# Kernel tuning notes

Hardware: AMD Instinct MI355X
Metric: run time of the kernel (lower is better)

## Reference

```python
import jax, jax.numpy as jnp
from jax import lax
import numpy as np

B, H, W = 128, 64, 64
L_I, L_H, L_Q, K = 3, 150, 16, 30
DN = ('NCHW', 'OIHW', 'NCHW')


def conv(x, w):
    return lax.conv_general_dilated(x, w, (1, 1), 'SAME', dimension_numbers=DN)


def setup_inputs() -> dict:
    key = jax.random.key(0)
    ks = jax.random.split(key, 10)
    return {
        'layout': jax.random.normal(ks[0], (B, 2, H, W), jnp.float32),
        'heatmap': jax.random.uniform(ks[1], (B, 1, H, W), jnp.float32),
        'h_w': jax.random.normal(ks[2], (L_H, L_I, 3, 3), jnp.float32) * 0.1,
        'h_b': jax.random.normal(ks[3], (L_H,), jnp.float32) * 0.1,
        'r_w': jax.random.normal(ks[4], (1, L_H, 1, 1), jnp.float32) * 0.1,
        'q_w': jax.random.normal(ks[5], (L_Q, 1, 3, 3), jnp.float32) * 0.1,
        'w': jax.random.normal(ks[6], (L_Q, 1, 3, 3), jnp.float32) * 0.1,
        'fc_w': jax.random.normal(ks[7], (4, L_Q), jnp.float32) * 0.1,
        'S1': jax.random.randint(ks[8], (B,), 0, H, jnp.int64),
        'S2': jax.random.randint(ks[9], (B,), 0, W, jnp.int64),
    }


def reference(layout, heatmap, h_w, h_b, r_w, q_w, w, fc_w, S1, S2):
    # X: [B, l_i, H, W]
    X = jnp.concatenate([layout, heatmap], axis=1)
    h = conv(X, h_w) + h_b[None, :, None, None]      # [B, l_h, H, W]
    r = conv(h, r_w)                                  # [B, 1, H, W]
    q = conv(r, q_w)                                  # [B, l_q, H, W]
    v = jnp.max(q, axis=1, keepdims=True)             # [B, 1, H, W]
    wq = jnp.concatenate([q_w, w], axis=1)            # [l_q, 2, 3, 3]

    def step(v, _):
        q = conv(jnp.concatenate([r, v], axis=1), wq)
        return jnp.max(q, axis=1, keepdims=True), None

    v, _ = lax.scan(step, v, None, length=K - 1)
    q = conv(jnp.concatenate([r, v], axis=1), wq)     # [B, l_q, H, W]

    b = jnp.arange(q.shape[0])
    q_out = q[b, :, S1, S2]                           # [B, l_q]
    logits = q_out @ fc_w.T                           # [B, 4]
    probs = jax.nn.softmax(logits, axis=-1)
    return logits, probs, v, r, heatmap
```

## Files before the change

kernel.cpp:

```cpp
#include <hip/hip_runtime.h>
#include <math.h>

#define NT 1024
#define PW 66
#define RR 52

template<int NIT, bool FIRST, bool LAST>
__global__ __launch_bounds__(NT)
__attribute__((amdgpu_waves_per_eu(4, 4)))
void vin_chunk(const float* __restrict__ layout,
               const float* __restrict__ heatmap,
               const float* __restrict__ h_w,
               const float* __restrict__ h_b,
               const float* __restrict__ r_w,
               const float* __restrict__ q_w,
               const float* __restrict__ w,
               const float* __restrict__ fc_w,
               const int* __restrict__ S1,
               const int* __restrict__ S2,
               float* __restrict__ vg,
               float* __restrict__ out)
{
    __shared__ float rh[28];
    __shared__ float r_s[RR * PW];
    __shared__ float va[RR * PW];
    __shared__ float vb[RR * PW];

    const int b2   = blockIdx.x;
    const int b    = b2 >> 1;
    const int half = b2 & 1;
    const int vlo  = half ? 16 : 0;
    const int tid  = threadIdx.x;

    for (int i = tid; i < RR * PW; i += NT) { r_s[i] = 0.f; va[i] = 0.f; vb[i] = 0.f; }
    __syncthreads();

    if (tid < 896) {
        const int coeff = tid >> 5, j = tid & 31;
        float s = 0.f;
        for (int c = j; c < 150; c += 32)
            s += r_w[c] * ((coeff < 27) ? h_w[c * 27 + coeff] : h_b[c]);
        s += __shfl_xor(s, 1, 32);  s += __shfl_xor(s, 2, 32);
        s += __shfl_xor(s, 4, 32);  s += __shfl_xor(s, 8, 32);
        s += __shfl_xor(s, 16, 32);
        if (j == 0) rh[coeff] = s;
    }
    const float* X0 = layout  + (size_t)b * 2 * 4096;
    const float* X1 = X0 + 4096;
    const float* X2 = heatmap + (size_t)b * 4096;
    for (int i = tid; i < RR * 64; i += NT) {
        const int M = i >> 6, col = i & 63;
        const int ir = vlo - 2 + M;
        if (ir >= 0 && ir < 64) {
            const int s = ir * 64 + col, d = M * PW + col + 1;
            r_s[d] = X0[s]; va[d] = X1[s]; vb[d] = X2[s];
        }
    }
    __syncthreads();

    float rv[4];
    int   rpx[4];
    #pragma unroll
    for (int k2 = 0; k2 < 4; ++k2) {
        const int i = tid + k2 * NT;
        rpx[k2] = -1;
        if (i < 50 * 64) {
            const int row = i >> 6, col = i & 63;
            float acc = rh[27];
            #pragma unroll
            for (int dy = 0; dy < 3; ++dy)
                #pragma unroll
                for (int dx = 0; dx < 3; ++dx) {
                    const int idx = (row + dy) * PW + col + dx;
                    acc = fmaf(rh[0 * 9 + dy * 3 + dx], r_s[idx], acc);
                    acc = fmaf(rh[1 * 9 + dy * 3 + dx], va[idx],  acc);
                    acc = fmaf(rh[2 * 9 + dy * 3 + dx], vb[idx],  acc);
                }
            const int ir = vlo - 1 + row;
            rv[k2]  = (ir >= 0 && ir < 64) ? acc : 0.f;
            rpx[k2] = row * PW + col + 1;
        }
    }
    __syncthreads();

    for (int i = tid; i < RR * PW; i += NT) { va[i] = 0.f; vb[i] = 0.f; }
    #pragma unroll
    for (int k2 = 0; k2 < 4; ++k2) if (rpx[k2] >= 0) r_s[rpx[k2]] = rv[k2];
    __syncthreads();

    const int wid  = tid >> 6, lane = tid & 63;
    const int g    = lane >> 4;
    const int p    = lane & 15;
    const int c    = (wid & 3) * 16 + p;
    const int band = wid >> 2;
    const int rb0  = band * 12;

    if (!FIRST) {
        for (int i = tid; i < 48 * 64; i += NT) {
            const int L = (i >> 6) + 1, col = i & 63;
            va[L * PW + col + 1] = vg[b * 4096 + (vlo + L - 1) * 64 + col];
        }
    }

    float wq[36];
    #pragma unroll
    for (int t = 0; t < 36; ++t) wq[t] = q_w[g * 36 + t];

    float rq[48];
    {
        const float* rw = r_s + rb0 * PW + c;
        float a0[3], a1[3], a2[3];
        #pragma unroll
        for (int d = 0; d < 3; ++d) { a0[d] = rw[d]; a1[d] = rw[PW + d]; }
        #pragma unroll
        for (int j = 0; j < 12; ++j) {
            #pragma unroll
            for (int d = 0; d < 3; ++d) a2[d] = rw[(j + 2) * PW + d];
            #pragma unroll
            for (int cc = 0; cc < 4; ++cc) {
                float a = 0.f;
                #pragma unroll
                for (int d = 0; d < 3; ++d) {
                    a = fmaf(wq[cc * 9 + d],     a0[d], a);
                    a = fmaf(wq[cc * 9 + 3 + d], a1[d], a);
                    a = fmaf(wq[cc * 9 + 6 + d], a2[d], a);
                }
                rq[cc * 12 + j] = a;
            }
            if (FIRST) {
                float m = fmaxf(fmaxf(rq[0 * 12 + j], rq[1 * 12 + j]),
                                fmaxf(rq[2 * 12 + j], rq[3 * 12 + j]));
                m = fmaxf(m, __shfl_xor(m, 16));
                m = fmaxf(m, __shfl_xor(m, 32));
                if (g == 0) va[(1 + rb0 + j) * PW + c + 1] = m;
            }
            #pragma unroll
            for (int d = 0; d < 3; ++d) { a0[d] = a1[d]; a1[d] = a2[d]; }
        }
    }

    float wv[36];
    #pragma unroll
    for (int t = 0; t < 36; ++t) wv[t] = w[g * 36 + t];
    __syncthreads();

    float* vcur = va;
    float* vnxt = vb;
    #pragma unroll 1
    for (int it = 0; it < NIT; ++it) {
        const float* vw = vcur + rb0 * PW + c;
        float a0[3], a1[3], a2[3];
        #pragma unroll
        for (int d = 0; d < 3; ++d) { a0[d] = vw[d]; a1[d] = vw[PW + d]; }
        #pragma unroll
        for (int j = 0; j < 12; ++j) {
            #pragma unroll
            for (int d = 0; d < 3; ++d) a2[d] = vw[(j + 2) * PW + d];
            float q0 = rq[0 * 12 + j], q1 = rq[1 * 12 + j];
            float q2 = rq[2 * 12 + j], q3 = rq[3 * 12 + j];
            #pragma unroll
            for (int d = 0; d < 3; ++d) {
                q0 = fmaf(wv[0 + d],  a0[d], q0); q0 = fmaf(wv[3 + d],  a1[d], q0); q0 = fmaf(wv[6 + d],  a2[d], q0);
                q1 = fmaf(wv[9 + d],  a0[d], q1); q1 = fmaf(wv[12 + d], a1[d], q1); q1 = fmaf(wv[15 + d], a2[d], q1);
                q2 = fmaf(wv[18 + d], a0[d], q2); q2 = fmaf(wv[21 + d], a1[d], q2); q2 = fmaf(wv[24 + d], a2[d], q2);
                q3 = fmaf(wv[27 + d], a0[d], q3); q3 = fmaf(wv[30 + d], a1[d], q3); q3 = fmaf(wv[33 + d], a2[d], q3);
            }
            float m = fmaxf(fmaxf(q0, q1), fmaxf(q2, q3));
            m = fmaxf(m, __shfl_xor(m, 16));
            m = fmaxf(m, __shfl_xor(m, 32));
            if (g == 0) vnxt[(1 + rb0 + j) * PW + c + 1] = m;
            #pragma unroll
            for (int d = 0; d < 3; ++d) { a0[d] = a1[d]; a1[d] = a2[d]; }
        }
        __syncthreads();
        float* t = vcur; vcur = vnxt; vnxt = t;
    }

    if (!LAST) {
        for (int i = tid; i < 32 * 64; i += NT) {
            const int ir = half * 32 + (i >> 6), col = i & 63;
            vg[b * 4096 + ir * 64 + col] = vcur[(ir - vlo + 1) * PW + col + 1];
        }
    } else {
        float* out_v = out + 1024 + (size_t)b * 4096;
        for (int i = tid; i < 32 * 64; i += NT) {
            const int ir = half * 32 + (i >> 6), col = i & 63;
            out_v[ir * 64 + col] = vcur[(ir - vlo + 1) * PW + col + 1];
        }
    }
    if (FIRST) {
        float* out_r = out + 1024 + (size_t)128 * 4096 + (size_t)b * 4096;
        float* out_h = out + 1024 + (size_t)256 * 4096 + (size_t)b * 4096;
        for (int i = tid; i < 32 * 64; i += NT) {
            const int ir = half * 32 + (i >> 6), col = i & 63;
            out_r[ir * 64 + col] = r_s[(ir - vlo + 1) * PW + col + 1];
            out_h[ir * 64 + col] = X2[ir * 64 + col];
        }
    }

    if (LAST) {
        const int s1 = S1[b], s2 = S2[b];
        if ((s1 >> 5) == half && tid == 0) {
            float q16[16];
            #pragma unroll
            for (int o = 0; o < 16; ++o) {
                float acc = 0.f;
                #pragma unroll
                for (int dy = 0; dy < 3; ++dy)
                    #pragma unroll
                    for (int dx = 0; dx < 3; ++dx) {
                        const int li = (s1 + dy - vlo) * PW + s2 + dx;
                        acc = fmaf(q_w[o * 9 + dy * 3 + dx], r_s[li], acc);
                        acc = fmaf(w[o * 9 + dy * 3 + dx],  vcur[li], acc);
                    }
                q16[o] = acc;
            }
            float lg[4];
            #pragma unroll
            for (int j = 0; j < 4; ++j) {
                float a = 0.f;
                #pragma unroll
                for (int o = 0; o < 16; ++o) a = fmaf(fc_w[j * 16 + o], q16[o], a);
                lg[j] = a;
            }
            const float m  = fmaxf(fmaxf(lg[0], lg[1]), fmaxf(lg[2], lg[3]));
            const float e0 = expf(lg[0] - m), e1 = expf(lg[1] - m);
            const float e2 = expf(lg[2] - m), e3 = expf(lg[3] - m);
            const float s  = e0 + e1 + e2 + e3;
            out[b * 4 + 0] = lg[0]; out[b * 4 + 1] = lg[1];
            out[b * 4 + 2] = lg[2]; out[b * 4 + 3] = lg[3];
            out[512 + b * 4 + 0] = e0 / s; out[512 + b * 4 + 1] = e1 / s;
            out[512 + b * 4 + 2] = e2 / s; out[512 + b * 4 + 3] = e3 / s;
        }
    }
}

extern "C" void kernel_launch(void* const* d_in, const int* in_sizes, int n_in,
                              void* d_out, int out_size, void* d_ws, size_t ws_size,
                              hipStream_t stream) {
    const float* layout  = (const float*)d_in[0];
    const float* heatmap = (const float*)d_in[1];
    const float* h_w     = (const float*)d_in[2];
    const float* h_b     = (const float*)d_in[3];
    const float* r_w     = (const float*)d_in[4];
    const float* q_w     = (const float*)d_in[5];
    const float* w       = (const float*)d_in[6];
    const float* fc_w    = (const float*)d_in[7];
    const int*   S1      = (const int*)d_in[8];
    const int*   S2      = (const int*)d_in[9];
    float* out = (float*)d_out;
    float* vg  = (float*)d_ws;

    hipLaunchKernelGGL((vin_chunk<15, true,  false>), dim3(256), dim3(NT), 0, stream,
                       layout, heatmap, h_w, h_b, r_w, q_w, w, fc_w, S1, S2, vg, out);
    hipLaunchKernelGGL((vin_chunk<14, false, true>),  dim3(256), dim3(NT), 0, stream,
                       layout, heatmap, h_w, h_b, r_w, q_w, w, fc_w, S1, S2, vg, out);
}
```

Measured before the change: 116.4 us.

## Split output channels across waves and reduce channel max via LDS atomicMax

Replaces the per-wave split of 16 output channels over lane groups with cross-wave shuffles by a scheme where each wave handles 8 channels for 64 columns and 6 rows. The channel max is combined across the two waves through LDS atomicMax on an order-preserving unsigned encoding of floats. Weights become wave-uniform via readfirstlane so they can sit in scalar registers. This needs triple-buffered value planes with per-iteration clearing, a wider padded row, and removal of the waves_per_eu hint. It trades shuffles and per-lane weight registers for LDS atomics and encode/decode overhead.

After: 137.0 us. +17.8%, slower.

```diff
diff --git a/kernel.cpp b/kernel.cpp
--- a/kernel.cpp
+++ b/kernel.cpp
@@ -2,12 +2,20 @@
 #include <math.h>
 
 #define NT 1024
-#define PW 66
+#define PW 68
 #define RR 52
+#define KB0 0x80000000u
+
+static __device__ __forceinline__ unsigned kenc(float f) {
+    unsigned u = __float_as_uint(f);
+    return ((int)u < 0) ? ~u : (u | 0x80000000u);
+}
+static __device__ __forceinline__ float kdec(unsigned k) {
+    return __uint_as_float((k & 0x80000000u) ? (k ^ 0x80000000u) : ~k);
+}
 
 template<int NIT, bool FIRST, bool LAST>
 __global__ __launch_bounds__(NT)
-__attribute__((amdgpu_waves_per_eu(4, 4)))
 void vin_chunk(const float* __restrict__ layout,
                const float* __restrict__ heatmap,
                const float* __restrict__ h_w,
@@ -21,10 +29,11 @@
                float* __restrict__ vg,
                float* __restrict__ out)
 {
-    __shared__ float rh[28];
-    __shared__ float r_s[RR * PW];
-    __shared__ float va[RR * PW];
-    __shared__ float vb[RR * PW];
+    __shared__ float    rh[28];
+    __shared__ float    r_s[RR * PW];
+    __shared__ unsigned va[RR * PW];
+    __shared__ unsigned vb[RR * PW];
+    __shared__ unsigned vc[RR * PW];
 
     const int b2   = blockIdx.x;
     const int b    = b2 >> 1;
@@ -32,14 +41,14 @@
     const int vlo  = half ? 16 : 0;
     const int tid  = threadIdx.x;
 
-    for (int i = tid; i < RR * PW; i += NT) { r_s[i] = 0.f; va[i] = 0.f; vb[i] = 0.f; }
+    for (int i = tid; i < RR * PW; i += NT) { r_s[i] = 0.f; va[i] = 0u; vb[i] = 0u; }
     __syncthreads();
 
     if (tid < 896) {
         const int coeff = tid >> 5, j = tid & 31;
         float s = 0.f;
-        for (int c = j; c < 150; c += 32)
-            s += r_w[c] * ((coeff < 27) ? h_w[c * 27 + coeff] : h_b[c]);
+        for (int cch = j; cch < 150; cch += 32)
+            s += r_w[cch] * ((coeff < 27) ? h_w[cch * 27 + coeff] : h_b[cch]);
         s += __shfl_xor(s, 1, 32);  s += __shfl_xor(s, 2, 32);
         s += __shfl_xor(s, 4, 32);  s += __shfl_xor(s, 8, 32);
         s += __shfl_xor(s, 16, 32);
@@ -52,8 +61,10 @@
         const int M = i >> 6, col = i & 63;
         const int ir = vlo - 2 + M;
         if (ir >= 0 && ir < 64) {
-            const int s = ir * 64 + col, d = M * PW + col + 1;
-            r_s[d] = X0[s]; va[d] = X1[s]; vb[d] = X2[s];
+            const int s = ir * 64 + col, d = M * PW + 2 + col;
+            r_s[d] = X0[s];
+            va[d]  = __float_as_uint(X1[s]);
+            vb[d]  = __float_as_uint(X2[s]);
         }
     }
     __syncthreads();
@@ -71,121 +82,128 @@
             for (int dy = 0; dy < 3; ++dy)
                 #pragma unroll
                 for (int dx = 0; dx < 3; ++dx) {
-                    const int idx = (row + dy) * PW + col + dx;
+                    const int idx = (row + dy) * PW + 1 + col + dx;
                     acc = fmaf(rh[0 * 9 + dy * 3 + dx], r_s[idx], acc);
-                    acc = fmaf(rh[1 * 9 + dy * 3 + dx], va[idx],  acc);
-                    acc = fmaf(rh[2 * 9 + dy * 3 + dx], vb[idx],  acc);
+                    acc = fmaf(rh[1 * 9 + dy * 3 + dx], __uint_as_float(va[idx]), acc);
+                    acc = fmaf(rh[2 * 9 + dy * 3 + dx], __uint_as_float(vb[idx]), acc);
                 }
             const int ir = vlo - 1 + row;
             rv[k2]  = (ir >= 0 && ir < 64) ? acc : 0.f;
-            rpx[k2] = row * PW + col + 1;
-        }
-    }
-    __syncthreads();
-
-    for (int i = tid; i < RR * PW; i += NT) { va[i] = 0.f; vb[i] = 0.f; }
+            rpx[k2] = row * PW + 2 + col;
+        }
+    }
+    __syncthreads();
+
+    for (int i = tid; i < 50 * PW; i += NT) {
+        const int row = i / PW, cc = i - row * PW;
+        const bool border = (row == 0) | (row == 49) | (cc < 2) | (cc > 65);
+        unsigned vav;
+        if (FIRST) vav = border ? KB0 : 0u;
+        else       vav = border ? KB0 : kenc(vg[b * 4096 + (vlo + row - 1) * 64 + (cc - 2)]);
+        va[i] = vav;
+        vb[i] = border ? KB0 : 0u;
+        vc[i] = border ? KB0 : 0u;
+    }
     #pragma unroll
     for (int k2 = 0; k2 < 4; ++k2) if (rpx[k2] >= 0) r_s[rpx[k2]] = rv[k2];
     __syncthreads();
 
     const int wid  = tid >> 6, lane = tid & 63;
-    const int g    = lane >> 4;
-    const int p    = lane & 15;
-    const int c    = (wid & 3) * 16 + p;
-    const int band = wid >> 2;
-    const int rb0  = band * 12;
-
-    if (!FIRST) {
-        for (int i = tid; i < 48 * 64; i += NT) {
-            const int L = (i >> 6) + 1, col = i & 63;
-            va[L * PW + col + 1] = vg[b * 4096 + (vlo + L - 1) * 64 + col];
-        }
-    }
-
-    float wq[36];
-    #pragma unroll
-    for (int t = 0; t < 36; ++t) wq[t] = q_w[g * 36 + t];
+    const int g2   = wid & 1;
+    const int band = wid >> 1;
+    const int rb0  = band * 6;
+    const int c    = lane;
+    const int gu   = __builtin_amdgcn_readfirstlane(g2);
 
     float rq[48];
     {
-        const float* rw = r_s + rb0 * PW + c;
+        float wqs[72];
+        #pragma unroll
+        for (int t = 0; t < 72; ++t)
+            wqs[t] = __int_as_float(__builtin_amdgcn_readfirstlane(
+                         __float_as_int(q_w[gu * 72 + t])));
         float a0[3], a1[3], a2[3];
         #pragma unroll
-        for (int d = 0; d < 3; ++d) { a0[d] = rw[d]; a1[d] = rw[PW + d]; }
-        #pragma unroll
-        for (int j = 0; j < 12; ++j) {
-            #pragma unroll
-            for (int d = 0; d < 3; ++d) a2[d] = rw[(j + 2) * PW + d];
-            #pragma unroll
-            for (int cc = 0; cc < 4; ++cc) {
-                float a = 0.f;
-                #pragma unroll
-                for (int d = 0; d < 3; ++d) {
-                    a = fmaf(wq[cc * 9 + d],     a0[d], a);
-                    a = fmaf(wq[cc * 9 + 3 + d], a1[d], a);
-                    a = fmaf(wq[cc * 9 + 6 + d], a2[d], a);
-                }
-                rq[cc * 12 + j] = a;
-            }
-            if (FIRST) {
-                float m = fmaxf(fmaxf(rq[0 * 12 + j], rq[1 * 12 + j]),
-                                fmaxf(rq[2 * 12 + j], rq[3 * 12 + j]));
-                m = fmaxf(m, __shfl_xor(m, 16));
-                m = fmaxf(m, __shfl_xor(m, 32));
-                if (g == 0) va[(1 + rb0 + j) * PW + c + 1] = m;
-            }
+        for (int d = 0; d < 3; ++d) {
+            a0[d] = r_s[rb0 * PW + 1 + c + d];
+            a1[d] = r_s[(rb0 + 1) * PW + 1 + c + d];
+        }
+        #pragma unroll
+        for (int j = 0; j < 6; ++j) {
+            #pragma unroll
+            for (int d = 0; d < 3; ++d) a2[d] = r_s[(rb0 + j + 2) * PW + 1 + c + d];
+            float m = 0.f;
+            #pragma unroll
+            for (int o = 0; o < 8; ++o) {
+                float q = 0.f;
+                q = fmaf(wqs[o*9+0], a0[0], q); q = fmaf(wqs[o*9+1], a0[1], q); q = fmaf(wqs[o*9+2], a0[2], q);
+                q = fmaf(wqs[o*9+3], a1[0], q); q = fmaf(wqs[o*9+4], a1[1], q); q = fmaf(wqs[o*9+5], a1[2], q);
+                q = fmaf(wqs[o*9+6], a2[0], q); q = fmaf(wqs[o*9+7], a2[1], q); q = fmaf(wqs[o*9+8], a2[2], q);
+                rq[o * 6 + j] = q;
+                m = (o == 0) ? q : fmaxf(m, q);
+            }
+            if (FIRST) atomicMax(&va[(rb0 + 1 + j) * PW + 2 + c], kenc(m));
             #pragma unroll
             for (int d = 0; d < 3; ++d) { a0[d] = a1[d]; a1[d] = a2[d]; }
         }
     }
 
-    float wv[36];
+    float wvs[72];
     #pragma unroll
-    for (int t = 0; t < 36; ++t) wv[t] = w[g * 36 + t];
-    __syncthreads();
-
-    float* vcur = va;
-    float* vnxt = vb;
+    for (int t = 0; t < 72; ++t)
+        wvs[t] = __int_as_float(__builtin_amdgcn_readfirstlane(
+                     __float_as_int(w[gu * 72 + t])));
+    __syncthreads();
+
+    unsigned* p0 = va;
+    unsigned* p1 = vb;
+    unsigned* p2 = vc;
+    uint2 z2; z2.x = 0u; z2.y = 0u;
     #pragma unroll 1
     for (int it = 0; it < NIT; ++it) {
-        const float* vw = vcur + rb0 * PW + c;
+        { const int t = tid;        const int row = (t >> 5) + 1, pr = t & 31;
+          *reinterpret_cast<uint2*>(&p2[row * PW + 2 + 2 * pr]) = z2; }
+        if (tid < 512) {
+          const int t = tid + 1024; const int row = (t >> 5) + 1, pr = t & 31;
+          *reinterpret_cast<uint2*>(&p2[row * PW + 2 + 2 * pr]) = z2; }
+
         float a0[3], a1[3], a2[3];
         #pragma unroll
-        for (int d = 0; d < 3; ++d) { a0[d] = vw[d]; a1[d] = vw[PW + d]; }
-        #pragma unroll
-        for (int j = 0; j < 12; ++j) {
-            #pragma unroll
-            for (int d = 0; d < 3; ++d) a2[d] = vw[(j + 2) * PW + d];
-            float q0 = rq[0 * 12 + j], q1 = rq[1 * 12 + j];
-            float q2 = rq[2 * 12 + j], q3 = rq[3 * 12 + j];
-            #pragma unroll
-            for (int d = 0; d < 3; ++d) {
-                q0 = fmaf(wv[0 + d],  a0[d], q0); q0 = fmaf(wv[3 + d],  a1[d], q0); q0 = fmaf(wv[6 + d],  a2[d], q0);
-                q1 = fmaf(wv[9 + d],  a0[d], q1); q1 = fmaf(wv[12 + d], a1[d], q1); q1 = fmaf(wv[15 + d], a2[d], q1);
-                q2 = fmaf(wv[18 + d], a0[d], q2); q2 = fmaf(wv[21 + d], a1[d], q2); q2 = fmaf(wv[24 + d], a2[d], q2);
-                q3 = fmaf(wv[27 + d], a0[d], q3); q3 = fmaf(wv[30 + d], a1[d], q3); q3 = fmaf(wv[33 + d], a2[d], q3);
-            }
-            float m = fmaxf(fmaxf(q0, q1), fmaxf(q2, q3));
-            m = fmaxf(m, __shfl_xor(m, 16));
-            m = fmaxf(m, __shfl_xor(m, 32));
-            if (g == 0) vnxt[(1 + rb0 + j) * PW + c + 1] = m;
+        for (int d = 0; d < 3; ++d) {
+            a0[d] = kdec(p0[rb0 * PW + 1 + c + d]);
+            a1[d] = kdec(p0[(rb0 + 1) * PW + 1 + c + d]);
+        }
+        #pragma unroll
+        for (int j = 0; j < 6; ++j) {
+            #pragma unroll
+            for (int d = 0; d < 3; ++d) a2[d] = kdec(p0[(rb0 + j + 2) * PW + 1 + c + d]);
+            float m = 0.f;
+            #pragma unroll
+            for (int o = 0; o < 8; ++o) {
+                float q = rq[o * 6 + j];
+                q = fmaf(wvs[o*9+0], a0[0], q); q = fmaf(wvs[o*9+1], a0[1], q); q = fmaf(wvs[o*9+2], a0[2], q);
+                q = fmaf(wvs[o*9+3], a1[0], q); q = fmaf(wvs[o*9+4], a1[1], q); q = fmaf(wvs[o*9+5], a1[2], q);
+                q = fmaf(wvs[o*9+6], a2[0], q); q = fmaf(wvs[o*9+7], a2[1], q); q = fmaf(wvs[o*9+8], a2[2], q);
+                m = (o == 0) ? q : fmaxf(m, q);
+            }
+            atomicMax(&p1[(rb0 + 1 + j) * PW + 2 + c], kenc(m));
             #pragma unroll
             for (int d = 0; d < 3; ++d) { a0[d] = a1[d]; a1[d] = a2[d]; }
         }
         __syncthreads();
-        float* t = vcur; vcur = vnxt; vnxt = t;
+        unsigned* tp = p0; p0 = p1; p1 = p2; p2 = tp;
     }
 
     if (!LAST) {
         for (int i = tid; i < 32 * 64; i += NT) {
             const int ir = half * 32 + (i >> 6), col = i & 63;
-            vg[b * 4096 + ir * 64 + col] = vcur[(ir - vlo + 1) * PW + col + 1];
+            vg[b * 4096 + ir * 64 + col] = kdec(p0[(ir - vlo + 1) * PW + 2 + col]);
         }
     } else {
         float* out_v = out + 1024 + (size_t)b * 4096;
         for (int i = tid; i < 32 * 64; i += NT) {
             const int ir = half * 32 + (i >> 6), col = i & 63;
-            out_v[ir * 64 + col] = vcur[(ir - vlo + 1) * PW + col + 1];
+            out_v[ir * 64 + col] = kdec(p0[(ir - vlo + 1) * PW + 2 + col]);
         }
     }
     if (FIRST) {
@@ -193,7 +211,7 @@
         float* out_h = out + 1024 + (size_t)256 * 4096 + (size_t)b * 4096;
         for (int i = tid; i < 32 * 64; i += NT) {
             const int ir = half * 32 + (i >> 6), col = i & 63;
-            out_r[ir * 64 + col] = r_s[(ir - vlo + 1) * PW + col + 1];
+            out_r[ir * 64 + col] = r_s[(ir - vlo + 1) * PW + 2 + col];
             out_h[ir * 64 + col] = X2[ir * 64 + col];
         }
     }
@@ -209,9 +227,9 @@
                 for (int dy = 0; dy < 3; ++dy)
                     #pragma unroll
                     for (int dx = 0; dx < 3; ++dx) {
-                        const int li = (s1 + dy - vlo) * PW + s2 + dx;
+                        const int li = (s1 + dy - vlo) * PW + 1 + s2 + dx;
                         acc = fmaf(q_w[o * 9 + dy * 3 + dx], r_s[li], acc);
-                        acc = fmaf(w[o * 9 + dy * 3 + dx],  vcur[li], acc);
+                        acc = fmaf(w[o * 9 + dy * 3 + dx],  kdec(p0[li]), acc);
                     }
                 q16[o] = acc;
             }
```

## Remap VI iteration so each thread computes all 16 channels for three rows

Applied to the files above, without the earlier changes.

The value-iteration and r-convolution stages are reorganised. Each thread now owns one column and three consecutive rows, and computes all 16 output channels itself with weights read from global/scalar memory. Previously each group of 4 lanes split the channels and combined results through cross-lane shuffles. This removes the shuffle reductions, cuts shared-memory reads per output (5x3 window loads for 3 rows), and drops the waves_per_eu attribute. In exchange each thread holds 48 rq registers plus more weight operands, which raises register pressure, and the amount of work per thread changes.

After: 140.6 us. +20.8%, slower.

```diff
diff --git a/kernel.cpp b/kernel.cpp
--- a/kernel.cpp
+++ b/kernel.cpp
@@ -7,7 +7,6 @@
 
 template<int NIT, bool FIRST, bool LAST>
 __global__ __launch_bounds__(NT)
-__attribute__((amdgpu_waves_per_eu(4, 4)))
 void vin_chunk(const float* __restrict__ layout,
                const float* __restrict__ heatmap,
                const float* __restrict__ h_w,
@@ -88,12 +87,9 @@
     for (int k2 = 0; k2 < 4; ++k2) if (rpx[k2] >= 0) r_s[rpx[k2]] = rv[k2];
     __syncthreads();
 
-    const int wid  = tid >> 6, lane = tid & 63;
-    const int g    = lane >> 4;
-    const int p    = lane & 15;
-    const int c    = (wid & 3) * 16 + p;
-    const int band = wid >> 2;
-    const int rb0  = band * 12;
+    const int c  = tid & 63;
+    const int ty = tid >> 6;
+    const int L0 = 1 + 3 * ty;
 
     if (!FIRST) {
         for (int i = tid; i < 48 * 64; i += NT) {
@@ -102,76 +98,60 @@
         }
     }
 
-    float wq[36];
-    #pragma unroll
-    for (int t = 0; t < 36; ++t) wq[t] = q_w[g * 36 + t];
-
-    float rq[48];
+    float rq[3][16];
     {
-        const float* rw = r_s + rb0 * PW + c;
-        float a0[3], a1[3], a2[3];
-        #pragma unroll
-        for (int d = 0; d < 3; ++d) { a0[d] = rw[d]; a1[d] = rw[PW + d]; }
-        #pragma unroll
-        for (int j = 0; j < 12; ++j) {
-            #pragma unroll
-            for (int d = 0; d < 3; ++d) a2[d] = rw[(j + 2) * PW + d];
-            #pragma unroll
-            for (int cc = 0; cc < 4; ++cc) {
-                float a = 0.f;
-                #pragma unroll
-                for (int d = 0; d < 3; ++d) {
-                    a = fmaf(wq[cc * 9 + d],     a0[d], a);
-                    a = fmaf(wq[cc * 9 + 3 + d], a1[d], a);
-                    a = fmaf(wq[cc * 9 + 6 + d], a2[d], a);
-                }
-                rq[cc * 12 + j] = a;
-            }
-            if (FIRST) {
-                float m = fmaxf(fmaxf(rq[0 * 12 + j], rq[1 * 12 + j]),
-                                fmaxf(rq[2 * 12 + j], rq[3 * 12 + j]));
-                m = fmaxf(m, __shfl_xor(m, 16));
-                m = fmaxf(m, __shfl_xor(m, 32));
-                if (g == 0) va[(1 + rb0 + j) * PW + c + 1] = m;
-            }
-            #pragma unroll
-            for (int d = 0; d < 3; ++d) { a0[d] = a1[d]; a1[d] = a2[d]; }
-        }
-    }
-
-    float wv[36];
-    #pragma unroll
-    for (int t = 0; t < 36; ++t) wv[t] = w[g * 36 + t];
+        float rn[5][3];
+        #pragma unroll
+        for (int i = 0; i < 5; ++i)
+            #pragma unroll
+            for (int d = 0; d < 3; ++d)
+                rn[i][d] = r_s[(3 * ty + i) * PW + c + d];
+        float m0[3];
+        #pragma unroll
+        for (int o = 0; o < 16; ++o) {
+            #pragma unroll
+            for (int j = 0; j < 3; ++j) {
+                float q = 0.f;
+                q = fmaf(q_w[o*9+0], rn[j+0][0], q); q = fmaf(q_w[o*9+1], rn[j+0][1], q); q = fmaf(q_w[o*9+2], rn[j+0][2], q);
+                q = fmaf(q_w[o*9+3], rn[j+1][0], q); q = fmaf(q_w[o*9+4], rn[j+1][1], q); q = fmaf(q_w[o*9+5], rn[j+1][2], q);
+                q = fmaf(q_w[o*9+6], rn[j+2][0], q); q = fmaf(q_w[o*9+7], rn[j+2][1], q); q = fmaf(q_w[o*9+8], rn[j+2][2], q);
+                rq[j][o] = q;
+                m0[j] = (o == 0) ? q : fmaxf(m0[j], q);
+            }
+        }
+        if (FIRST) {
+            #pragma unroll
+            for (int j = 0; j < 3; ++j)
+                va[(L0 + j) * PW + c + 1] = m0[j];
+        }
+    }
     __syncthreads();
 
     float* vcur = va;
     float* vnxt = vb;
     #pragma unroll 1
     for (int it = 0; it < NIT; ++it) {
-        const float* vw = vcur + rb0 * PW + c;
-        float a0[3], a1[3], a2[3];
-        #pragma unroll
-        for (int d = 0; d < 3; ++d) { a0[d] = vw[d]; a1[d] = vw[PW + d]; }
-        #pragma unroll
-        for (int j = 0; j < 12; ++j) {
-            #pragma unroll
-            for (int d = 0; d < 3; ++d) a2[d] = vw[(j + 2) * PW + d];
-            float q0 = rq[0 * 12 + j], q1 = rq[1 * 12 + j];
-            float q2 = rq[2 * 12 + j], q3 = rq[3 * 12 + j];
-            #pragma unroll
-            for (int d = 0; d < 3; ++d) {
-                q0 = fmaf(wv[0 + d],  a0[d], q0); q0 = fmaf(wv[3 + d],  a1[d], q0); q0 = fmaf(wv[6 + d],  a2[d], q0);
-                q1 = fmaf(wv[9 + d],  a0[d], q1); q1 = fmaf(wv[12 + d], a1[d], q1); q1 = fmaf(wv[15 + d], a2[d], q1);
-                q2 = fmaf(wv[18 + d], a0[d], q2); q2 = fmaf(wv[21 + d], a1[d], q2); q2 = fmaf(wv[24 + d], a2[d], q2);
-                q3 = fmaf(wv[27 + d], a0[d], q3); q3 = fmaf(wv[30 + d], a1[d], q3); q3 = fmaf(wv[33 + d], a2[d], q3);
-            }
-            float m = fmaxf(fmaxf(q0, q1), fmaxf(q2, q3));
-            m = fmaxf(m, __shfl_xor(m, 16));
-            m = fmaxf(m, __shfl_xor(m, 32));
-            if (g == 0) vnxt[(1 + rb0 + j) * PW + c + 1] = m;
-            #pragma unroll
-            for (int d = 0; d < 3; ++d) { a0[d] = a1[d]; a1[d] = a2[d]; }
-        }
+        float vn[5][3];
+        #pragma unroll
+        for (int i = 0; i < 5; ++i)
+            #pragma unroll
+            for (int d = 0; d < 3; ++d)
+                vn[i][d] = vcur[(3 * ty + i) * PW + c + d];
+        float m[3];
+        #pragma unroll
+        for (int o = 0; o < 16; ++o) {
+            #pragma unroll
+            for (int j = 0; j < 3; ++j) {
+                float q = rq[j][o];
+                q = fmaf(w[o*9+0], vn[j+0][0], q); q = fmaf(w[o*9+1], vn[j+0][1], q); q = fmaf(w[o*9+2], vn[j+0][2], q);
+                q = fmaf(w[o*9+3], vn[j+1][0], q); q = fmaf(w[o*9+4], vn[j+1][1], q); q = fmaf(w[o*9+5], vn[j+1][2], q);
+                q = fmaf(w[o*9+6], vn[j+2][0], q); q = fmaf(w[o*9+7], vn[j+2][1], q); q = fmaf(w[o*9+8], vn[j+2][2], q);
+                m[j] = (o == 0) ? q : fmaxf(m[j], q);
+            }
+        }
+        #pragma unroll
+        for (int j = 0; j < 3; ++j)
+            vnxt[(L0 + j) * PW + c + 1] = m[j];
         __syncthreads();
         float* t = vcur; vcur = vnxt; vnxt = t;
     }
```
